# Optimization experiments

Hardware: AMD Instinct MI355X
Metric: run time of the kernel (lower is better)

Reference implementation:

```python
import jax, jax.numpy as jnp
import numpy as np

B, H, N, D, T = 4, 16, 1024, 64, 4

def setup_inputs() -> dict:
    key = jax.random.key(0)
    kq, kk, kv, ka, kw = jax.random.split(key, 5)
    Q = jax.random.normal(kq, (B, H, N, D), dtype=jnp.float32)
    K = jax.random.normal(kk, (B, H, N, D), dtype=jnp.float32)
    V = jax.random.normal(kv, (B, H, N, D), dtype=jnp.float32)
    # stacked adjacency matrices, one [B, N, N] per edge type
    A = jax.random.uniform(ka, (T, B, N, N), dtype=jnp.float32)
    # per-edge-type, per-head learned scalar bias weights (glorot-init scalars in torch)
    weight_E = jax.random.normal(kw, (T, H), dtype=jnp.float32)
    return {"Q": Q, "K": K, "V": V, "A": A, "weight_E": weight_E}

def reference(Q, K, V, A, weight_E):
    scale = Q.shape[-1] ** 0.5
    # raw scores [B, H, N, N]
    attn_score = jnp.einsum("bhnd,bhmd->bhnm", Q, K)
    # B_E = sum_t attn_score * (A_t * w_t)  ->  attn_score * sum_t (A_t * w_t)
    bias_factor = jnp.einsum("tbnm,th->bhnm", A, weight_E)
    attn_score = (attn_score + attn_score * bias_factor) / scale
    attn_weight = jax.nn.softmax(attn_score, axis=-1)
    out = jnp.einsum("bhnm,bhmd->bhnd", attn_weight, V)  # dropout p=0.0 is identity
    return out, attn_weight
```

## Files before the change

kernel.cpp:

```cpp
#include <hip/hip_runtime.h>


#define NB 4
#define NH 16
#define NN 1024
#define ND 64
#define NT 4

typedef short s16x4 __attribute__((ext_vector_type(4)));
typedef short s16x8 __attribute__((ext_vector_type(8)));
typedef float f32x4 __attribute__((ext_vector_type(4)));

__device__ __forceinline__ short f2bf(float f) {
  return __builtin_bit_cast(short, (__bf16)f);
}
__device__ __forceinline__ float bf2f(short s) {
  return __builtin_bit_cast(float, ((unsigned)(unsigned short)s) << 16);
}

__device__ __forceinline__ void gload_lds16(const void* g, void* l) {
  __builtin_amdgcn_global_load_lds(
      (const __attribute__((address_space(1))) unsigned int*)g,
      (__attribute__((address_space(3))) unsigned int*)l, 16, 0, 0);
}

__global__ void pack_k(const float* __restrict__ Kg, short* __restrict__ Khi,
                       short* __restrict__ Klo) {
  int t = blockIdx.x * 256 + threadIdx.x;
  int p0 = t * 8;
  int bh = p0 >> 16;
  int rem = p0 & 65535;
  int chunk = rem >> 12;
  int e = rem & 4095;
  int r = e >> 6;
  int dd0 = e & 63;
  int d0 = dd0 ^ ((r & 7) << 3);
  const float* src = Kg + ((size_t)bh * NN + chunk * 64 + r) * ND + d0;
  float4 a = *reinterpret_cast<const float4*>(src);
  float4 c4 = *reinterpret_cast<const float4*>(src + 4);
  float f[8] = {a.x, a.y, a.z, a.w, c4.x, c4.y, c4.z, c4.w};
  s16x8 hi, lo;
#pragma unroll
  for (int j = 0; j < 8; ++j) {
    short h = f2bf(f[j]);
    hi[j] = h;
    lo[j] = f2bf(f[j] - bf2f(h));
  }
  *reinterpret_cast<s16x8*>(Khi + p0) = hi;
  *reinterpret_cast<s16x8*>(Klo + p0) = lo;
}

__global__ void pack_vt(const float* __restrict__ Vg, short* __restrict__ Vt) {
  __shared__ float tile[64 * 65];
  int bh = blockIdx.x >> 4;
  int kc = blockIdx.x & 15;
  int tid = threadIdx.x;
#pragma unroll
  for (int i = 0; i < 4; ++i) {
    int e = tid + i * 256;
    int k = e >> 4, d0 = (e & 15) * 4;
    const float* src = Vg + ((size_t)bh * NN + kc * 64 + k) * ND + d0;
    float4 v = *reinterpret_cast<const float4*>(src);
    float* dst = &tile[k * 65 + d0];
    dst[0] = v.x; dst[1] = v.y; dst[2] = v.z; dst[3] = v.w;
  }
  __syncthreads();
  {
    int d = tid >> 2;
    int kk = (tid & 3) * 16;
    s16x8 o0, o1;
#pragma unroll
    for (int j = 0; j < 8; ++j) o0[j] = f2bf(tile[(kk + j) * 65 + d]);
#pragma unroll
    for (int j = 0; j < 8; ++j) o1[j] = f2bf(tile[(kk + 8 + j) * 65 + d]);
    short* dst = Vt + ((size_t)bh * ND + d) * NN + kc * 64 + kk;
    *reinterpret_cast<s16x8*>(dst) = o0;
    *reinterpret_cast<s16x8*>(dst + 8) = o1;
  }
}

__global__ __launch_bounds__(256, 3) void mrsa_main(
    const float* __restrict__ Qg, const float* __restrict__ Ag,
    const float* __restrict__ Wg, const short* __restrict__ Khi,
    const short* __restrict__ Klo, const short* __restrict__ Vt,
    float* __restrict__ outO, float* __restrict__ outW) {
  __shared__ short kbuf[16384];
  __shared__ float red0[16][4];
  __shared__ float red1[16][4];

  const int tid = threadIdx.x;
  const int lane = tid & 63;
  const int wv = tid >> 6;
  const int l4 = lane & 15;
  const int hi4 = lane >> 4;

  const int x = blockIdx.x & 7;
  const int i = blockIdx.x >> 3;
  const int b = x >> 1;
  const int h = ((i >> 5) & 1) * 8 + (i & 7);
  const int rb = (x & 1) * 32 + ((i >> 6) << 2) + ((i >> 3) & 3);
  const int row0 = rb * 16;

  const size_t bh = (size_t)b * NH + h;
  const float* Qp = Qg + bh * (NN * ND);

  float wE[NT];
#pragma unroll
  for (int t = 0; t < NT; ++t) wE[t] = Wg[t * NH + h];

  const int k0 = hi4 * 8;

  s16x8 qh[2], ql[2];
#pragma unroll
  for (int ks = 0; ks < 2; ++ks) {
    const float* qrow = Qp + (size_t)(row0 + l4) * ND + ks * 32 + k0;
#pragma unroll
    for (int j = 0; j < 8; ++j) {
      float f = qrow[j];
      short hb = f2bf(f);
      qh[ks][j] = hb;
      ql[ks][j] = f2bf(f - bf2f(hb));
    }
  }

  const int bcol = wv * 16 + l4;
  const int bsw = (bcol & 7) << 3;
  const size_t kbase = bh * 65536;

  const float* Ap[NT];
#pragma unroll
  for (int t = 0; t < NT; ++t)
    Ap[t] = Ag + ((size_t)t * NB + b) * (NN * NN) +
            (size_t)(row0 + hi4 * 4) * NN + bcol;

  f32x4 sAcc[16];
  float aBuf[2][NT][4];

#define STAGE_K(cc)                                                         \
  do {                                                                      \
    size_t g0 =                                                             \
        kbase + (size_t)(cc)*4096 + (size_t)wv * 1024 + (size_t)lane * 8;   \
    short* KH = &kbuf[((cc)&1) * 8192];                                     \
    short* KL = KH + 4096;                                                  \
    gload_lds16(Khi + g0, KH + wv * 1024);                                  \
    gload_lds16(Khi + g0 + 512, KH + wv * 1024 + 512);                      \
    gload_lds16(Klo + g0, KL + wv * 1024);                                  \
    gload_lds16(Klo + g0 + 512, KL + wv * 1024 + 512);                      \
  } while (0)

#define ISSUE_A(cc)                                                         \
  do {                                                                      \
    _Pragma("unroll") for (int t = 0; t < NT; ++t) {                        \
      _Pragma("unroll") for (int r = 0; r < 4; ++r) {                       \
        aBuf[(cc)&1][t][r] = Ap[t][r * NN + (cc)*64];                       \
      }                                                                     \
    }                                                                       \
  } while (0)

  STAGE_K(0);
  ISSUE_A(0);

#pragma unroll
  for (int c = 0; c < 16; ++c) {
    __syncthreads();
    if (c < 15) {
      STAGE_K(c + 1);
      ISSUE_A(c + 1);
    }
    const short* KH = &kbuf[(c & 1) * 8192];
    const short* KL = KH + 4096;
    s16x8 kh8[2], kl8[2];
#pragma unroll
    for (int ks = 0; ks < 2; ++ks) {
      int ph = bcol * 64 + ((ks * 32 + k0) ^ bsw);
      kh8[ks] = *reinterpret_cast<const s16x8*>(&KH[ph]);
      kl8[ks] = *reinterpret_cast<const s16x8*>(&KL[ph]);
    }
    f32x4 acc = {0.f, 0.f, 0.f, 0.f};
#pragma unroll
    for (int ks = 0; ks < 2; ++ks) {
      acc = __builtin_amdgcn_mfma_f32_16x16x32_bf16(qh[ks], kh8[ks], acc, 0, 0, 0);
      acc = __builtin_amdgcn_mfma_f32_16x16x32_bf16(qh[ks], kl8[ks], acc, 0, 0, 0);
      acc = __builtin_amdgcn_mfma_f32_16x16x32_bf16(ql[ks], kh8[ks], acc, 0, 0, 0);
    }
#pragma unroll
    for (int r = 0; r < 4; ++r) {
      float bias = wE[0] * aBuf[c & 1][0][r] + wE[1] * aBuf[c & 1][1][r] +
                   wE[2] * aBuf[c & 1][2][r] + wE[3] * aBuf[c & 1][3][r];
      sAcc[c][r] = acc[r] * (1.f + bias) * 0.125f;
    }
  }

  float mr[4];
#pragma unroll
  for (int r = 0; r < 4; ++r) {
    float m = sAcc[0][r];
#pragma unroll
    for (int c = 1; c < 16; ++c) m = fmaxf(m, sAcc[c][r]);
    mr[r] = m;
  }
#pragma unroll
  for (int off = 8; off >= 1; off >>= 1) {
#pragma unroll
    for (int r = 0; r < 4; ++r) mr[r] = fmaxf(mr[r], __shfl_xor(mr[r], off));
  }
  if (l4 == 0) {
#pragma unroll
    for (int r = 0; r < 4; ++r) red0[hi4 * 4 + r][wv] = mr[r];
  }
  __syncthreads();
  float mfin[4], inv[4];
#pragma unroll
  for (int r = 0; r < 4; ++r) {
    float4 v = *reinterpret_cast<const float4*>(&red0[hi4 * 4 + r][0]);
    mfin[r] = fmaxf(fmaxf(v.x, v.y), fmaxf(v.z, v.w));
  }
  float sr[4];
#pragma unroll
  for (int r = 0; r < 4; ++r) {
    float s = 0.f;
#pragma unroll
    for (int c = 0; c < 16; ++c) {
      float e = __expf(sAcc[c][r] - mfin[r]);
      sAcc[c][r] = e;
      s += e;
    }
    sr[r] = s;
  }
#pragma unroll
  for (int off = 8; off >= 1; off >>= 1) {
#pragma unroll
    for (int r = 0; r < 4; ++r) sr[r] += __shfl_xor(sr[r], off);
  }
  if (l4 == 0) {
#pragma unroll
    for (int r = 0; r < 4; ++r) red1[hi4 * 4 + r][wv] = sr[r];
  }
  __syncthreads();
#pragma unroll
  for (int r = 0; r < 4; ++r) {
    float4 v = *reinterpret_cast<const float4*>(&red1[hi4 * 4 + r][0]);
    inv[r] = 1.f / (v.x + v.y + v.z + v.w);
  }

#pragma unroll
  for (int r = 0; r < 4; ++r) {
    const int lrow = hi4 * 4 + r;
    const int prow = lrow * 1024;
    const int swc = bcol ^ ((lrow & 7) << 3);
#pragma unroll
    for (int c = 0; c < 16; ++c) {
      kbuf[prow + c * 64 + swc] = f2bf(sAcc[c][r] * inv[r]);
    }
  }
  __syncthreads();

  {
    f32x4 acc = {0.f, 0.f, 0.f, 0.f};
    const int dcol = bcol;
    const int abase = l4 * 1024;
    const int asw = (l4 & 7) << 3;
    const short* vtp = Vt + (bh * ND + (size_t)dcol) * NN;
#pragma unroll 8
    for (int kk = 0; kk < 32; ++kk) {
      int kb = kk * 32 + k0;
      s16x8 af = *reinterpret_cast<const s16x8*>(&kbuf[abase + (kb ^ asw)]);
      s16x8 bfv = *reinterpret_cast<const s16x8*>(&vtp[kb]);
      acc = __builtin_amdgcn_mfma_f32_16x16x32_bf16(af, bfv, acc, 0, 0, 0);
    }
#pragma unroll
    for (int r = 0; r < 4; ++r) {
      __builtin_nontemporal_store(
          acc[r], &outO[(bh * NN + (size_t)(row0 + hi4 * 4 + r)) * ND + dcol]);
    }
  }

#pragma unroll
  for (int rr = 0; rr < 4; ++rr) {
    const int row = wv * 4 + rr;
    const int sw8 = (row & 7) << 3;
    float* gw = outW + ((bh * NN + (size_t)(row0 + row)) << 10);
    const int prow = row * 1024;
#pragma unroll
    for (int i2 = 0; i2 < 4; ++i2) {
      int gcol = lane * 4 + i2 * 256;
      s16x4 p4 = *reinterpret_cast<const s16x4*>(&kbuf[prow + (gcol ^ sw8)]);
      f32x4 w4;
      w4[0] = bf2f(p4[0]);
      w4[1] = bf2f(p4[1]);
      w4[2] = bf2f(p4[2]);
      w4[3] = bf2f(p4[3]);
      __builtin_nontemporal_store(w4, reinterpret_cast<f32x4*>(&gw[gcol]));
    }
  }
#undef STAGE_K
#undef ISSUE_A
}

__global__ __launch_bounds__(256, 2) void mrsa_fused(
    const float* __restrict__ Qg, const float* __restrict__ Kg,
    const float* __restrict__ Vg, const float* __restrict__ Ag,
    const float* __restrict__ Wg, float* __restrict__ outO,
    float* __restrict__ outW) {
  __shared__ short KsHi[64 * 64];
  __shared__ short KsLo[64 * 64];
  __shared__ float Ss[16 * 1024];
  const int tid = threadIdx.x;
  const int lane = tid & 63;
  const int wv = tid >> 6;
  const int rb = blockIdx.x;
  const int h = blockIdx.y;
  const int b = blockIdx.z;
  const int row0 = rb * 16;
  const size_t bh = (size_t)b * NH + h;
  const float* Qp = Qg + bh * (NN * ND);
  const float* Kp = Kg + bh * (NN * ND);
  const float* Vp = Vg + bh * (NN * ND);
  float wE[NT];
#pragma unroll
  for (int t = 0; t < NT; ++t) wE[t] = Wg[t * NH + h];
  const int arow = lane & 15;
  const int k0 = (lane >> 4) * 8;
  s16x8 qh[2], ql[2];
#pragma unroll
  for (int ks = 0; ks < 2; ++ks) {
    const float* qrow = Qp + (size_t)(row0 + arow) * ND + ks * 32 + k0;
#pragma unroll
    for (int j = 0; j < 8; ++j) {
      float f = qrow[j];
      short hi = f2bf(f);
      qh[ks][j] = hi;
      ql[ks][j] = f2bf(f - bf2f(hi));
    }
  }
  const int bcol = wv * 16 + (lane & 15);
  const int bsw = (bcol & 7) << 3;
  for (int c = 0; c < 16; ++c) {
#pragma unroll
    for (int i = 0; i < 4; ++i) {
      int e4 = tid + i * 256;
      int r = e4 >> 4;
      int d0 = (e4 & 15) * 4;
      float4 kv = *reinterpret_cast<const float4*>(
          Kp + (size_t)(c * 64 + r) * ND + d0);
      float kf[4];
      kf[0] = kv.x; kf[1] = kv.y; kf[2] = kv.z; kf[3] = kv.w;
      s16x4 hi4, lo4;
#pragma unroll
      for (int j = 0; j < 4; ++j) {
        short hi = f2bf(kf[j]);
        hi4[j] = hi;
        lo4[j] = f2bf(kf[j] - bf2f(hi));
      }
      int sw = r * 64 + (d0 ^ ((r & 7) << 3));
      *reinterpret_cast<s16x4*>(&KsHi[sw]) = hi4;
      *reinterpret_cast<s16x4*>(&KsLo[sw]) = lo4;
    }
    __syncthreads();
    f32x4 acc = {0.f, 0.f, 0.f, 0.f};
#pragma unroll
    for (int ks = 0; ks < 2; ++ks) {
      int kb = ks * 32 + k0;
      int ph = bcol * 64 + (kb ^ bsw);
      s16x8 kh8 = *reinterpret_cast<const s16x8*>(&KsHi[ph]);
      s16x8 kl8 = *reinterpret_cast<const s16x8*>(&KsLo[ph]);
      acc = __builtin_amdgcn_mfma_f32_16x16x32_bf16(qh[ks], kh8, acc, 0, 0, 0);
      acc = __builtin_amdgcn_mfma_f32_16x16x32_bf16(qh[ks], kl8, acc, 0, 0, 0);
      acc = __builtin_amdgcn_mfma_f32_16x16x32_bf16(ql[ks], kh8, acc, 0, 0, 0);
    }
    int gcol = c * 64 + bcol;
#pragma unroll
    for (int r = 0; r < 4; ++r) {
      int lrow = (lane >> 4) * 4 + r;
      int grow = row0 + lrow;
      float bias = 0.f;
#pragma unroll
      for (int t = 0; t < NT; ++t)
        bias += wE[t] *
                Ag[((size_t)t * NB + b) * (NN * NN) + (size_t)grow * NN + gcol];
      Ss[lrow * 1024 + (gcol ^ ((lrow & 7) << 3))] =
          acc[r] * (1.f + bias) * 0.125f;
    }
    __syncthreads();
  }
#pragma unroll
  for (int rr = 0; rr < 4; ++rr) {
    int lrow = wv * 4 + rr;
    float* srow = &Ss[lrow * 1024];
    int sw = (lrow & 7) << 3;
    float m = -3.4e38f;
#pragma unroll
    for (int i = 0; i < 16; ++i) m = fmaxf(m, srow[i * 64 + lane]);
#pragma unroll
    for (int off = 32; off; off >>= 1) m = fmaxf(m, __shfl_xor(m, off));
    float ev[16];
    float lsum = 0.f;
#pragma unroll
    for (int i = 0; i < 16; ++i) {
      float e = __expf(srow[i * 64 + lane] - m);
      ev[i] = e;
      lsum += e;
    }
#pragma unroll
    for (int off = 32; off; off >>= 1) lsum += __shfl_xor(lsum, off);
    float inv = 1.f / lsum;
    float* gw = outW + (bh * NN + (size_t)(row0 + lrow)) * NN;
#pragma unroll
    for (int i = 0; i < 16; ++i) {
      float w = ev[i] * inv;
      int p = i * 64 + lane;
      srow[p] = w;
      gw[p ^ sw] = w;
    }
  }
  __syncthreads();
  {
    f32x4 acc = {0.f, 0.f, 0.f, 0.f};
    const int dcol = wv * 16 + (lane & 15);
    const int asw = (arow & 7) << 3;
    const float* srow = &Ss[arow * 1024];
#pragma unroll 2
    for (int kk = 0; kk < 32; ++kk) {
      int kb = kk * 32 + k0;
      int ph = kb ^ asw;
      float4 a0 = *reinterpret_cast<const float4*>(&srow[ph]);
      float4 a1 = *reinterpret_cast<const float4*>(&srow[ph + 4]);
      s16x8 af, bfv;
      af[0] = f2bf(a0.x); af[1] = f2bf(a0.y);
      af[2] = f2bf(a0.z); af[3] = f2bf(a0.w);
      af[4] = f2bf(a1.x); af[5] = f2bf(a1.y);
      af[6] = f2bf(a1.z); af[7] = f2bf(a1.w);
      const float* vcol = Vp + (size_t)kb * ND + dcol;
#pragma unroll
      for (int j = 0; j < 8; ++j) bfv[j] = f2bf(vcol[j * ND]);
      acc = __builtin_amdgcn_mfma_f32_16x16x32_bf16(af, bfv, acc, 0, 0, 0);
    }
#pragma unroll
    for (int r = 0; r < 4; ++r) {
      int lrow = (lane >> 4) * 4 + r;
      outO[(bh * NN + (size_t)(row0 + lrow)) * ND + dcol] = acc[r];
    }
  }
}

extern "C" void kernel_launch(void* const* d_in, const int* in_sizes, int n_in,
                              void* d_out, int out_size, void* d_ws,
                              size_t ws_size, hipStream_t stream) {
  const float* Q = (const float*)d_in[0];
  const float* K = (const float*)d_in[1];
  const float* V = (const float*)d_in[2];
  const float* A = (const float*)d_in[3];
  const float* wE = (const float*)d_in[4];
  float* out = (float*)d_out;
  float* outW = out + (size_t)NB * NH * NN * ND;

  const size_t nElem = (size_t)NB * NH * NN * ND;
  const size_t needK = 3 * nElem * sizeof(short);
  if (ws_size >= needK) {
    short* Khi = (short*)d_ws;
    short* Klo = Khi + nElem;
    short* Vt = Klo + nElem;
    hipLaunchKernelGGL(pack_k, dim3(2048), dim3(256), 0, stream, K, Khi, Klo);
    hipLaunchKernelGGL(pack_vt, dim3(NB * NH * 16), dim3(256), 0, stream, V,
                       Vt);
    hipLaunchKernelGGL(mrsa_main, dim3(4096), dim3(256), 0, stream, Q, A, wE,
                       Khi, Klo, Vt, out, outW);
  } else {
    dim3 grid(NN / 16, NH, NB);
    hipLaunchKernelGGL(mrsa_fused, grid, dim3(256), 0, stream, Q, K, V, A, wE,
                       out, outW);
  }
}
```

Before: 185.8 us.

## Transpose QK MFMA output so each lane owns one row, vectorizing A loads

Swaps the MFMA operand order so the score tile comes out transposed: each lane holds four consecutive key columns of a single query row. The adjacency loads become one float4 per edge type instead of four strided scalar loads. Row max and sum now need only two cross-lane shuffles and a single LDS slot per lane. Probabilities are written to LDS as packed 4-element bf16 vectors rather than scalar shorts. The swizzle indexing and the remaining softmax and PV logic have to stay consistent with the new per-lane ownership.

```diff
diff --git a/kernel.cpp b/kernel.cpp
--- a/kernel.cpp
+++ b/kernel.cpp
@@ -127,14 +127,15 @@
   const int bsw = (bcol & 7) << 3;
   const size_t kbase = bh * 65536;
 
+  const int mbase = wv * 16 + hi4 * 4;
   const float* Ap[NT];
 #pragma unroll
   for (int t = 0; t < NT; ++t)
     Ap[t] = Ag + ((size_t)t * NB + b) * (NN * NN) +
-            (size_t)(row0 + hi4 * 4) * NN + bcol;
+            (size_t)(row0 + l4) * NN + mbase;
 
   f32x4 sAcc[16];
-  float aBuf[2][NT][4];
+  float4 aB4[2][NT];
 
 #define STAGE_K(cc)                                                         \
   do {                                                                      \
@@ -151,9 +152,8 @@
 #define ISSUE_A(cc)                                                         \
   do {                                                                      \
     _Pragma("unroll") for (int t = 0; t < NT; ++t) {                        \
-      _Pragma("unroll") for (int r = 0; r < 4; ++r) {                       \
-        aBuf[(cc)&1][t][r] = Ap[t][r * NN + (cc)*64];                       \
-      }                                                                     \
+      aB4[(cc)&1][t] =                                                      \
+          *reinterpret_cast<const float4*>(Ap[t] + (cc)*64);                \
     }                                                                       \
   } while (0)
 
@@ -179,85 +179,74 @@
     f32x4 acc = {0.f, 0.f, 0.f, 0.f};
 #pragma unroll
     for (int ks = 0; ks < 2; ++ks) {
-      acc = __builtin_amdgcn_mfma_f32_16x16x32_bf16(qh[ks], kh8[ks], acc, 0, 0, 0);
-      acc = __builtin_amdgcn_mfma_f32_16x16x32_bf16(qh[ks], kl8[ks], acc, 0, 0, 0);
-      acc = __builtin_amdgcn_mfma_f32_16x16x32_bf16(ql[ks], kh8[ks], acc, 0, 0, 0);
-    }
+      acc = __builtin_amdgcn_mfma_f32_16x16x32_bf16(kh8[ks], qh[ks], acc, 0, 0, 0);
+      acc = __builtin_amdgcn_mfma_f32_16x16x32_bf16(kl8[ks], qh[ks], acc, 0, 0, 0);
+      acc = __builtin_amdgcn_mfma_f32_16x16x32_bf16(kh8[ks], ql[ks], acc, 0, 0, 0);
+    }
+    float4 a0 = aB4[c & 1][0], a1 = aB4[c & 1][1];
+    float4 a2 = aB4[c & 1][2], a3 = aB4[c & 1][3];
+    float b0 = wE[0] * a0.x + wE[1] * a1.x + wE[2] * a2.x + wE[3] * a3.x;
+    float b1 = wE[0] * a0.y + wE[1] * a1.y + wE[2] * a2.y + wE[3] * a3.y;
+    float b2 = wE[0] * a0.z + wE[1] * a1.z + wE[2] * a2.z + wE[3] * a3.z;
+    float b3 = wE[0] * a0.w + wE[1] * a1.w + wE[2] * a2.w + wE[3] * a3.w;
+    sAcc[c][0] = acc[0] * (1.f + b0) * 0.125f;
+    sAcc[c][1] = acc[1] * (1.f + b1) * 0.125f;
+    sAcc[c][2] = acc[2] * (1.f + b2) * 0.125f;
+    sAcc[c][3] = acc[3] * (1.f + b3) * 0.125f;
+  }
+
+  float m = sAcc[0][0];
+#pragma unroll
+  for (int c = 0; c < 16; ++c) {
+#pragma unroll
+    for (int r = 0; r < 4; ++r) m = fmaxf(m, sAcc[c][r]);
+  }
+  m = fmaxf(m, __shfl_xor(m, 16));
+  m = fmaxf(m, __shfl_xor(m, 32));
+  if (hi4 == 0) red0[l4][wv] = m;
+  __syncthreads();
+  float mfin, inv;
+  {
+    float4 v = *reinterpret_cast<const float4*>(&red0[l4][0]);
+    mfin = fmaxf(fmaxf(v.x, v.y), fmaxf(v.z, v.w));
+  }
+  float s = 0.f;
+#pragma unroll
+  for (int c = 0; c < 16; ++c) {
 #pragma unroll
     for (int r = 0; r < 4; ++r) {
-      float bias = wE[0] * aBuf[c & 1][0][r] + wE[1] * aBuf[c & 1][1][r] +
-                   wE[2] * aBuf[c & 1][2][r] + wE[3] * aBuf[c & 1][3][r];
-      sAcc[c][r] = acc[r] * (1.f + bias) * 0.125f;
-    }
-  }
-
-  float mr[4];
-#pragma unroll
-  for (int r = 0; r < 4; ++r) {
-    float m = sAcc[0][r];
-#pragma unroll
-    for (int c = 1; c < 16; ++c) m = fmaxf(m, sAcc[c][r]);
-    mr[r] = m;
-  }
-#pragma unroll
-  for (int off = 8; off >= 1; off >>= 1) {
-#pragma unroll
-    for (int r = 0; r < 4; ++r) mr[r] = fmaxf(mr[r], __shfl_xor(mr[r], off));
-  }
-  if (l4 == 0) {
-#pragma unroll
-    for (int r = 0; r < 4; ++r) red0[hi4 * 4 + r][wv] = mr[r];
-  }
-  __syncthreads();
-  float mfin[4], inv[4];
-#pragma unroll
-  for (int r = 0; r < 4; ++r) {
-    float4 v = *reinterpret_cast<const float4*>(&red0[hi4 * 4 + r][0]);
-    mfin[r] = fmaxf(fmaxf(v.x, v.y), fmaxf(v.z, v.w));
-  }
-  float sr[4];
-#pragma unroll
-  for (int r = 0; r < 4; ++r) {
-    float s = 0.f;
-#pragma unroll
-    for (int c = 0; c < 16; ++c) {
-      float e = __expf(sAcc[c][r] - mfin[r]);
+      float e = __expf(sAcc[c][r] - mfin);
       sAcc[c][r] = e;
       s += e;
     }
-    sr[r] = s;
-  }
-#pragma unroll
-  for (int off = 8; off >= 1; off >>= 1) {
-#pragma unroll
-    for (int r = 0; r < 4; ++r) sr[r] += __shfl_xor(sr[r], off);
-  }
-  if (l4 == 0) {
-#pragma unroll
-    for (int r = 0; r < 4; ++r) red1[hi4 * 4 + r][wv] = sr[r];
-  }
+  }
+  s += __shfl_xor(s, 16);
+  s += __shfl_xor(s, 32);
+  if (hi4 == 0) red1[l4][wv] = s;
   __syncthreads();
-#pragma unroll
-  for (int r = 0; r < 4; ++r) {
-    float4 v = *reinterpret_cast<const float4*>(&red1[hi4 * 4 + r][0]);
-    inv[r] = 1.f / (v.x + v.y + v.z + v.w);
-  }
-
-#pragma unroll
-  for (int r = 0; r < 4; ++r) {
-    const int lrow = hi4 * 4 + r;
-    const int prow = lrow * 1024;
-    const int swc = bcol ^ ((lrow & 7) << 3);
+  {
+    float4 v = *reinterpret_cast<const float4*>(&red1[l4][0]);
+    inv = 1.f / (v.x + v.y + v.z + v.w);
+  }
+
+  {
+    const int prow = l4 * 1024;
+    const int swz = (l4 & 7) << 3;
 #pragma unroll
     for (int c = 0; c < 16; ++c) {
-      kbuf[prow + c * 64 + swc] = f2bf(sAcc[c][r] * inv[r]);
+      s16x4 p;
+      p[0] = f2bf(sAcc[c][0] * inv);
+      p[1] = f2bf(sAcc[c][1] * inv);
+      p[2] = f2bf(sAcc[c][2] * inv);
+      p[3] = f2bf(sAcc[c][3] * inv);
+      *reinterpret_cast<s16x4*>(&kbuf[prow + ((c * 64 + mbase) ^ swz)]) = p;
     }
   }
   __syncthreads();
 
   {
     f32x4 acc = {0.f, 0.f, 0.f, 0.f};
-    const int dcol = bcol;
+    const int dcol = wv * 16 + l4;
     const int abase = l4 * 1024;
     const int asw = (l4 & 7) << 3;
     const short* vtp = Vt + (bh * ND + (size_t)dcol) * NN;
```

Result: slower. 239.1 us (+28.7%).
